# Performance work log

Hardware: AMD Instinct MI355X
Metric: run time of the kernel (lower is better)

The kernel has to match this reference:

```python
import jax, jax.numpy as jnp
import numpy as np

DIM = 1024
DEPTH = 2
HEADS = 16
DH = 64
INNER = HEADS * DH  # == DIM
MLP = 4096
B, N, M = 2, 1024, 1024
EPS = 1e-5
SCALE = DH ** -0.5


def _ln(x, g, b):
    mu = x.mean(-1, keepdims=True)
    var = ((x - mu) ** 2).mean(-1, keepdims=True)
    return (x - mu) / jnp.sqrt(var + EPS) * g + b


def _split_heads(t):  # [b, n, inner] -> [b, h, n, d]
    b, n, _ = t.shape
    return t.reshape(b, n, HEADS, DH).transpose(0, 2, 1, 3)


def _merge_heads(t):  # [b, h, n, d] -> [b, n, inner]
    b, h, n, d = t.shape
    return t.transpose(0, 2, 1, 3).reshape(b, n, h * d)


def _mha(q, k, v):
    dots = jnp.einsum('bhnd,bhmd->bhnm', q, k) * SCALE
    attn = jax.nn.softmax(dots, axis=-1)
    return jnp.einsum('bhnm,bhmd->bhnd', attn, v)


def setup_inputs() -> dict:
    key = jax.random.key(0)
    ks = jax.random.split(key, 12)
    rn = lambda k, shape, s=0.02: jax.random.normal(k, shape, dtype=jnp.float32) * s
    return {
        'x': rn(ks[0], (B, N, DIM), 1.0),
        'context': rn(ks[1], (B, M, DIM), 1.0),
        'ln1_g': jnp.ones((DEPTH, DIM), jnp.float32),
        'ln1_b': jnp.zeros((DEPTH, DIM), jnp.float32),
        'w_qkv': rn(ks[2], (DEPTH, DIM, 3 * INNER)),
        'w_o1': rn(ks[3], (DEPTH, INNER, DIM)),
        'b_o1': jnp.zeros((DEPTH, DIM), jnp.float32),
        'ln2_g': jnp.ones((DEPTH, DIM), jnp.float32),
        'ln2_b': jnp.zeros((DEPTH, DIM), jnp.float32),
        'w_q': rn(ks[4], (DEPTH, DIM, INNER)),
        'w_k': rn(ks[5], (DEPTH, DIM, INNER)),
        'w_v': rn(ks[6], (DEPTH, DIM, INNER)),
        'w_o2': rn(ks[7], (DEPTH, INNER, DIM)),
        'b_o2': jnp.zeros((DEPTH, DIM), jnp.float32),
        'ln3_g': jnp.ones((DEPTH, DIM), jnp.float32),
        'ln3_b': jnp.zeros((DEPTH, DIM), jnp.float32),
        'w_ff1': rn(ks[8], (DEPTH, DIM, MLP)),
        'b_ff1': jnp.zeros((DEPTH, MLP), jnp.float32),
        'w_ff2': rn(ks[9], (DEPTH, MLP, DIM)),
        'b_ff2': jnp.zeros((DEPTH, DIM), jnp.float32),
    }


def reference(x, context, ln1_g, ln1_b, w_qkv, w_o1, b_o1, ln2_g, ln2_b,
              w_q, w_k, w_v, w_o2, b_o2, ln3_g, ln3_b,
              w_ff1, b_ff1, w_ff2, b_ff2):
    for l in range(DEPTH):
        # PreNorm self-attention + residual
        h = _ln(x, ln1_g[l], ln1_b[l])
        qkv = h @ w_qkv[l]
        q, k, v = jnp.split(qkv, 3, axis=-1)
        out = _merge_heads(_mha(_split_heads(q), _split_heads(k), _split_heads(v)))
        x = out @ w_o1[l] + b_o1[l] + x
        # PreNorm cross-attention (context is NOT normed, matching PreNorm) + residual
        h = _ln(x, ln2_g[l], ln2_b[l])
        q2 = _split_heads(h @ w_q[l])
        k2 = _split_heads(context @ w_k[l])
        v2 = _split_heads(context @ w_v[l])
        out = _merge_heads(_mha(q2, k2, v2))
        x = out @ w_o2[l] + b_o2[l] + x
        # PreNorm FFN (exact GELU, matching nn.GELU default) + residual
        h = _ln(x, ln3_g[l], ln3_b[l])
        h = jax.nn.gelu(h @ w_ff1[l] + b_ff1[l], approximate=False)
        x = h @ w_ff2[l] + b_ff2[l] + x
    return x
```

## Files before the change

### kernel.cpp

```cpp
#include <hip/hip_runtime.h>

typedef __attribute__((ext_vector_type(8))) short bf16x8;
typedef __attribute__((ext_vector_type(4))) short short4v;
typedef __attribute__((ext_vector_type(4))) float f32x4;

__device__ __forceinline__ float bf2f(short s) {
    union { unsigned u; float f; } c;
    c.u = ((unsigned)(unsigned short)s) << 16;
    return c.f;
}
__device__ __forceinline__ short f2bf(float f) {
    union { float f; unsigned u; } c; c.f = f;
    unsigned r = (c.u + 0x7fffu + ((c.u >> 16) & 1u)) >> 16;
    return (short)r;
}

#define AS1(p) ((__attribute__((address_space(1))) void*)(void*)(p))
#define AS3(p) ((__attribute__((address_space(3))) void*)(p))

template<int MODE, int BM>
__global__ __launch_bounds__(256) void gemm_bt(
    const short* __restrict__ A, int lda,
    const short* __restrict__ B, int ldb,
    void* __restrict__ Cv, int ldc,
    const float* __restrict__ bias, const float* __restrict__ resid,
    int M, int N, int K, int ntn, float scale)
{
    constexpr int MF = (BM == 128) ? 4 : 2;
    __shared__ short As[BM * 32];
    __shared__ short Bs[128 * 32];

    const int tm = (blockIdx.x / ntn) * BM;
    const int tn = (blockIdx.x % ntn) * 128;

    const int tid = threadIdx.x;
    const int w = tid >> 6, l = tid & 63;
    const int lane16 = l & 15, kg = l >> 4;
    const int wr = (BM == 128) ? (w >> 1) * 64 : (w & 1) * 32;
    const int wc = (BM == 128) ? (w & 1) * 64 : (w >> 1) * 64;

    f32x4 acc[MF][4] = {};

    for (int k0 = 0; k0 < K; k0 += 32) {
        if constexpr (BM == 128) {
            const int lr = l >> 2, lc = l & 3;
            #pragma unroll
            for (int i = 0; i < 2; ++i) {
                int row = (i * 4 + w) * 16 + lr;
                int ga = tm + row; if (ga > M - 1) ga = M - 1;
                const short* srca = A + (long)ga * lda + k0 + lc * 8;
                __builtin_amdgcn_global_load_lds(AS1(srca), AS3(As + (i * 4 + w) * 512), 16, 0, 0);
                int gb = tn + row; if (gb > N - 1) gb = N - 1;
                const short* srcb = B + (long)gb * ldb + k0 + lc * 8;
                __builtin_amdgcn_global_load_lds(AS1(srcb), AS3(Bs + (i * 4 + w) * 512), 16, 0, 0);
            }
        } else {
            const int lr = l >> 2, lc = l & 3;
            {
                int row = w * 16 + lr;
                int ga = tm + row; if (ga > M - 1) ga = M - 1;
                const short* srca = A + (long)ga * lda + k0 + lc * 8;
                __builtin_amdgcn_global_load_lds(AS1(srca), AS3(As + w * 512), 16, 0, 0);
            }
            #pragma unroll
            for (int i = 0; i < 2; ++i) {
                int row = i * 64 + w * 16 + lr;
                int gb = tn + row; if (gb > N - 1) gb = N - 1;
                const short* srcb = B + (long)gb * ldb + k0 + lc * 8;
                __builtin_amdgcn_global_load_lds(AS1(srcb), AS3(Bs + i * 2048 + w * 512), 16, 0, 0);
            }
        }
        __syncthreads();

        bf16x8 af[MF], bfr[4];
        #pragma unroll
        for (int m = 0; m < MF; ++m)
            af[m] = *(const bf16x8*)(As + (wr + m * 16 + lane16) * 32 + kg * 8);
        #pragma unroll
        for (int n = 0; n < 4; ++n)
            bfr[n] = *(const bf16x8*)(Bs + (wc + n * 16 + lane16) * 32 + kg * 8);
        #pragma unroll
        for (int m = 0; m < MF; ++m)
            #pragma unroll
            for (int n = 0; n < 4; ++n)
                acc[m][n] = __builtin_amdgcn_mfma_f32_16x16x32_bf16(af[m], bfr[n], acc[m][n], 0, 0, 0);
        __syncthreads();
    }

    if (MODE == 2) {
        float* C = (float*)Cv;
        #pragma unroll
        for (int m = 0; m < MF; ++m)
            #pragma unroll
            for (int n = 0; n < 4; ++n) {
                int col = tn + wc + n * 16 + lane16;
                if (col >= N) continue;
                #pragma unroll
                for (int r = 0; r < 4; ++r) {
                    int row = tm + wr + m * 16 + kg * 4 + r;
                    if (row >= M) continue;
                    long idx = (long)row * ldc + col;
                    C[idx] = acc[m][n][r] * scale + bias[col] + resid[idx];
                }
            }
    } else {
        short* C = (short*)Cv;
        #pragma unroll
        for (int m = 0; m < MF; ++m)
            #pragma unroll
            for (int n = 0; n < 4; ++n) {
                int col = tn + wc + n * 16 + lane16;
                if (col >= N) continue;
                #pragma unroll
                for (int r = 0; r < 4; ++r) {
                    int row = tm + wr + m * 16 + kg * 4 + r;
                    if (row >= M) continue;
                    float v = acc[m][n][r] * scale;
                    if (MODE == 1) {
                        v += bias[col];
                        v = 0.5f * v * (1.0f + erff(v * 0.7071067811865476f));
                    }
                    C[(long)row * ldc + col] = f2bf(v);
                }
            }
    }
}

__global__ __launch_bounds__(512) void flash_attn(
    const short* __restrict__ Q, int ldq, long sQb,
    const short* __restrict__ K, int ldk, long sKb,
    const short* __restrict__ Vt,
    short* __restrict__ O, int ldo, long sOb)
{
    __shared__ short Ks[2][64 * 64];
    __shared__ short Vts[2][64 * 64];
    __shared__ short Ps[8][16 * 72];

    const int z = blockIdx.x;
    const int b = z >> 4, h = z & 15;
    const int qt = blockIdx.y;

    const int tid = threadIdx.x;
    const int w = tid >> 6, l = tid & 63;
    const int lane16 = l & 15, kg = l >> 4;

    const short* Qg = Q + sQb * b + h * 64;
    const short* Kg = K + sKb * b + h * 64;
    const short* Vtg = Vt + (long)z * 65536;
    short* Og = O + sOb * b + h * 64 + (long)(qt * 128 + w * 16) * ldo;

    const int srow = w * 8 + (l >> 3);
    const int schunk = (l & 7) ^ (srow & 7);

    bf16x8 aq[2];
    {
        const short* qp = Qg + (long)(qt * 128 + w * 16 + lane16) * ldq + kg * 8;
        aq[0] = *(const bf16x8*)(qp);
        aq[1] = *(const bf16x8*)(qp + 32);
    }

    f32x4 acc_o[4] = {};
    float m_run[4], l_run[4];
    #pragma unroll
    for (int r = 0; r < 4; ++r) { m_run[r] = -1e30f; l_run[r] = 0.f; }

    short* Pw = (short*)Ps + w * (16 * 72);

    {
        const short* srck = Kg + (long)srow * ldk + schunk * 8;
        __builtin_amdgcn_global_load_lds(AS1(srck), AS3((short*)Ks + w * 512), 16, 0, 0);
        const short* srcv = Vtg + (long)srow * 1024 + schunk * 8;
        __builtin_amdgcn_global_load_lds(AS1(srcv), AS3((short*)Vts + w * 512), 16, 0, 0);
    }

    int cur = 0;
    for (int t = 0; t < 16; ++t) {
        __syncthreads();
        if (t < 15) {
            const short* srck = Kg + (long)((t + 1) * 64 + srow) * ldk + schunk * 8;
            __builtin_amdgcn_global_load_lds(AS1(srck), AS3((short*)Ks + (cur ^ 1) * 4096 + w * 512), 16, 0, 0);
            const short* srcv = Vtg + (long)srow * 1024 + (t + 1) * 64 + schunk * 8;
            __builtin_amdgcn_global_load_lds(AS1(srcv), AS3((short*)Vts + (cur ^ 1) * 4096 + w * 512), 16, 0, 0);
        }
        const short* Kb = (const short*)Ks + cur * 4096;
        const short* Vb = (const short*)Vts + cur * 4096;

        f32x4 acc_s[4] = {};
        #pragma unroll
        for (int n = 0; n < 4; ++n) {
            int row = 16 * n + lane16;
            #pragma unroll
            for (int ks = 0; ks < 2; ++ks) {
                bf16x8 bk = *(const bf16x8*)(Kb + row * 64 + (((ks * 4 + kg) ^ (row & 7)) * 8));
                acc_s[n] = __builtin_amdgcn_mfma_f32_16x16x32_bf16(aq[ks], bk, acc_s[n], 0, 0, 0);
            }
        }

        float mt[4], p[4][4], rs[4], mnew[4], corr[4];
        #pragma unroll
        for (int n = 0; n < 4; ++n)
            #pragma unroll
            for (int r = 0; r < 4; ++r) acc_s[n][r] *= 0.125f;
        #pragma unroll
        for (int r = 0; r < 4; ++r)
            mt[r] = fmaxf(fmaxf(acc_s[0][r], acc_s[1][r]), fmaxf(acc_s[2][r], acc_s[3][r]));
        #pragma unroll
        for (int off = 1; off < 16; off <<= 1)
            #pragma unroll
            for (int r = 0; r < 4; ++r) mt[r] = fmaxf(mt[r], __shfl_xor(mt[r], off));
        #pragma unroll
        for (int r = 0; r < 4; ++r) {
            mnew[r] = fmaxf(m_run[r], mt[r]);
            corr[r] = __expf(m_run[r] - mnew[r]);
            m_run[r] = mnew[r];
            rs[r] = 0.f;
        }
        #pragma unroll
        for (int n = 0; n < 4; ++n)
            #pragma unroll
            for (int r = 0; r < 4; ++r) {
                float e = __expf(acc_s[n][r] - mnew[r]);
                p[n][r] = e; rs[r] += e;
            }
        #pragma unroll
        for (int off = 1; off < 16; off <<= 1)
            #pragma unroll
            for (int r = 0; r < 4; ++r) rs[r] += __shfl_xor(rs[r], off);
        #pragma unroll
        for (int r = 0; r < 4; ++r) {
            l_run[r] = l_run[r] * corr[r] + rs[r];
            #pragma unroll
            for (int nd = 0; nd < 4; ++nd) acc_o[nd][r] *= corr[r];
        }

        #pragma unroll
        for (int n = 0; n < 4; ++n)
            #pragma unroll
            for (int r = 0; r < 4; ++r)
                Pw[(kg * 4 + r) * 72 + 16 * n + lane16] = f2bf(p[n][r]);

        #pragma unroll
        for (int kk = 0; kk < 2; ++kk) {
            bf16x8 pa = *(const bf16x8*)(Pw + lane16 * 72 + kk * 32 + kg * 8);
            #pragma unroll
            for (int nd = 0; nd < 4; ++nd) {
                int d = 16 * nd + lane16;
                bf16x8 bv = *(const bf16x8*)(Vb + d * 64 + (((kk * 4 + kg) ^ (d & 7)) * 8));
                acc_o[nd] = __builtin_amdgcn_mfma_f32_16x16x32_bf16(pa, bv, acc_o[nd], 0, 0, 0);
            }
        }
        cur ^= 1;
    }

    #pragma unroll
    for (int r = 0; r < 4; ++r) {
        float inv = 1.0f / l_run[r];
        #pragma unroll
        for (int nd = 0; nd < 4; ++nd)
            Og[(long)(kg * 4 + r) * ldo + nd * 16 + lane16] = f2bf(acc_o[nd][r] * inv);
    }
}

__global__ __launch_bounds__(256) void ln_bf16(const float* __restrict__ x,
                                               const float* __restrict__ g,
                                               const float* __restrict__ b,
                                               short* __restrict__ h)
{
    const long row = blockIdx.x;
    const int tid = threadIdx.x;
    float4 v = ((const float4*)(x + row * 1024))[tid];
    float s  = v.x + v.y + v.z + v.w;
    float s2 = v.x * v.x + v.y * v.y + v.z * v.z + v.w * v.w;
    #pragma unroll
    for (int off = 1; off < 64; off <<= 1) {
        s  += __shfl_xor(s, off);
        s2 += __shfl_xor(s2, off);
    }
    __shared__ float rs[4], rs2[4];
    int w = tid >> 6;
    if ((tid & 63) == 0) { rs[w] = s; rs2[w] = s2; }
    __syncthreads();
    s  = rs[0] + rs[1] + rs[2] + rs[3];
    s2 = rs2[0] + rs2[1] + rs2[2] + rs2[3];
    float mu  = s * (1.0f / 1024.0f);
    float var = s2 * (1.0f / 1024.0f) - mu * mu;
    float inv = rsqrtf(var + 1e-5f);
    float4 gv = ((const float4*)g)[tid];
    float4 bv = ((const float4*)b)[tid];
    short4v o;
    o[0] = f2bf((v.x - mu) * inv * gv.x + bv.x);
    o[1] = f2bf((v.y - mu) * inv * gv.y + bv.y);
    o[2] = f2bf((v.z - mu) * inv * gv.z + bv.z);
    o[3] = f2bf((v.w - mu) * inv * gv.w + bv.w);
    ((short4v*)(h + row * 1024))[tid] = o;
}

__global__ __launch_bounds__(256) void wconv_t(const float* __restrict__ in,
                                               short* __restrict__ out, int R, int C)
{
    __shared__ float t[32][33];
    const int c0 = blockIdx.x * 32, r0 = blockIdx.y * 32;
    const int tx = threadIdx.x & 31, ty = threadIdx.x >> 5;
    #pragma unroll
    for (int i = 0; i < 4; ++i)
        t[ty + i * 8][tx] = in[(long)(r0 + ty + i * 8) * C + c0 + tx];
    __syncthreads();
    #pragma unroll
    for (int i = 0; i < 4; ++i)
        out[(long)(c0 + ty + i * 8) * R + r0 + tx] = f2bf(t[tx][ty + i * 8]);
}

__global__ __launch_bounds__(256) void vtrans(const short* __restrict__ src, int ld, int col_off,
                                              short* __restrict__ vt)
{
    __shared__ short t[32][33];
    const int z = blockIdx.z, bb = z >> 4, hh = z & 15;
    const int m0 = blockIdx.x * 32, d0 = blockIdx.y * 32;
    const int tx = threadIdx.x & 31, ty = threadIdx.x >> 5;
    const short* sp = src + (long)(bb * 1024) * ld + col_off + hh * 64;
    #pragma unroll
    for (int i = 0; i < 4; ++i)
        t[ty + i * 8][tx] = sp[(long)(m0 + ty + i * 8) * ld + d0 + tx];
    __syncthreads();
    short* op = vt + (long)z * 64 * 1024;
    #pragma unroll
    for (int i = 0; i < 4; ++i)
        op[(long)(d0 + ty + i * 8) * 1024 + m0 + tx] = t[tx][ty + i * 8];
}

__global__ __launch_bounds__(256) void f2bf_vec(const float* __restrict__ in,
                                                short* __restrict__ out, int n4)
{
    int i = blockIdx.x * 256 + threadIdx.x;
    if (i < n4) {
        float4 v = ((const float4*)in)[i];
        short4v o;
        o[0] = f2bf(v.x); o[1] = f2bf(v.y); o[2] = f2bf(v.z); o[3] = f2bf(v.w);
        ((short4v*)out)[i] = o;
    }
}

template<int MODE, int BM>
static void launch_gemm(const short* A, int lda, const short* B, int ldb,
                        void* C, int ldc, const float* bias, const float* resid,
                        int M, int N, int K, float scale, hipStream_t stream)
{
    int ntm = (M + BM - 1) / BM, ntn = (N + 127) / 128;
    dim3 grid(ntm * ntn);
    gemm_bt<MODE, BM><<<grid, 256, 0, stream>>>(A, lda, B, ldb, C, ldc, bias, resid,
                                                M, N, K, ntn, scale);
}

extern "C" void kernel_launch(void* const* d_in, const int* in_sizes, int n_in,
                              void* d_out, int out_size, void* d_ws, size_t ws_size,
                              hipStream_t stream)
{
    const float* x_in  = (const float*)d_in[0];
    const float* ctx   = (const float*)d_in[1];
    const float* ln1_g = (const float*)d_in[2];
    const float* ln1_b = (const float*)d_in[3];
    const float* w_qkv = (const float*)d_in[4];
    const float* w_o1  = (const float*)d_in[5];
    const float* b_o1  = (const float*)d_in[6];
    const float* ln2_g = (const float*)d_in[7];
    const float* ln2_b = (const float*)d_in[8];
    const float* w_q   = (const float*)d_in[9];
    const float* w_k   = (const float*)d_in[10];
    const float* w_v   = (const float*)d_in[11];
    const float* w_o2  = (const float*)d_in[12];
    const float* b_o2  = (const float*)d_in[13];
    const float* ln3_g = (const float*)d_in[14];
    const float* ln3_b = (const float*)d_in[15];
    const float* w_ff1 = (const float*)d_in[16];
    const float* b_ff1 = (const float*)d_in[17];
    const float* w_ff2 = (const float*)d_in[18];
    const float* b_ff2 = (const float*)d_in[19];
    float* xo = (float*)d_out;

    char* p = (char*)d_ws;
    short* wbuf   = (short*)(p);
    short* hbuf   = (short*)(p + 8388608);
    short* qkvbuf = (short*)(p + 12582912);
    short* vt     = (short*)(p + 92274688);
    short* aout   = (short*)(p + 96468992);
    short* ffbuf  = (short*)(p + 100663296);
    short* ctxbuf = (short*)(p + 117440512);

    hipMemcpyAsync(xo, x_in, (size_t)2 * 1024 * 1024 * 4, hipMemcpyDeviceToDevice, stream);
    f2bf_vec<<<2048, 256, 0, stream>>>(ctx, ctxbuf, 2 * 1024 * 1024 / 4);

    for (int l = 0; l < 2; ++l) {
        ln_bf16<<<2048, 256, 0, stream>>>(xo, ln1_g + l * 1024, ln1_b + l * 1024, hbuf);
        wconv_t<<<dim3(96, 32), 256, 0, stream>>>(w_qkv + (long)l * 1024 * 3072, wbuf, 1024, 3072);
        launch_gemm<0, 128>(hbuf, 1024, wbuf, 1024, qkvbuf, 3072,
                            nullptr, nullptr, 2048, 3072, 1024, 1.0f, stream);
        vtrans<<<dim3(32, 2, 32), 256, 0, stream>>>(qkvbuf, 3072, 2048, vt);
        flash_attn<<<dim3(32, 8), 512, 0, stream>>>(qkvbuf, 3072, 3145728L,
                                                    qkvbuf + 1024, 3072, 3145728L,
                                                    vt, aout, 1024, 1048576L);
        wconv_t<<<dim3(32, 32), 256, 0, stream>>>(w_o1 + (long)l * 1048576, wbuf, 1024, 1024);
        launch_gemm<2, 64>(aout, 1024, wbuf, 1024, xo, 1024,
                           b_o1 + l * 1024, xo, 2048, 1024, 1024, 1.0f, stream);

        ln_bf16<<<2048, 256, 0, stream>>>(xo, ln2_g + l * 1024, ln2_b + l * 1024, hbuf);
        short* q2 = qkvbuf;
        short* k2 = qkvbuf + 2048 * 1024;
        short* v2 = qkvbuf + 2 * 2048 * 1024;
        wconv_t<<<dim3(32, 32), 256, 0, stream>>>(w_q + (long)l * 1048576, wbuf, 1024, 1024);
        launch_gemm<0, 64>(hbuf, 1024, wbuf, 1024, q2, 1024,
                           nullptr, nullptr, 2048, 1024, 1024, 1.0f, stream);
        wconv_t<<<dim3(32, 32), 256, 0, stream>>>(w_k + (long)l * 1048576, wbuf, 1024, 1024);
        launch_gemm<0, 64>(ctxbuf, 1024, wbuf, 1024, k2, 1024,
                           nullptr, nullptr, 2048, 1024, 1024, 1.0f, stream);
        wconv_t<<<dim3(32, 32), 256, 0, stream>>>(w_v + (long)l * 1048576, wbuf, 1024, 1024);
        launch_gemm<0, 64>(ctxbuf, 1024, wbuf, 1024, v2, 1024,
                           nullptr, nullptr, 2048, 1024, 1024, 1.0f, stream);
        vtrans<<<dim3(32, 2, 32), 256, 0, stream>>>(v2, 1024, 0, vt);
        flash_attn<<<dim3(32, 8), 512, 0, stream>>>(q2, 1024, 1048576L,
                                                    k2, 1024, 1048576L,
                                                    vt, aout, 1024, 1048576L);
        wconv_t<<<dim3(32, 32), 256, 0, stream>>>(w_o2 + (long)l * 1048576, wbuf, 1024, 1024);
        launch_gemm<2, 64>(aout, 1024, wbuf, 1024, xo, 1024,
                           b_o2 + l * 1024, xo, 2048, 1024, 1024, 1.0f, stream);

        ln_bf16<<<2048, 256, 0, stream>>>(xo, ln3_g + l * 1024, ln3_b + l * 1024, hbuf);
        wconv_t<<<dim3(128, 32), 256, 0, stream>>>(w_ff1 + (long)l * 1024 * 4096, wbuf, 1024, 4096);
        launch_gemm<1, 128>(hbuf, 1024, wbuf, 1024, ffbuf, 4096,
                            b_ff1 + l * 4096, nullptr, 2048, 4096, 1024, 1.0f, stream);
        wconv_t<<<dim3(32, 128), 256, 0, stream>>>(w_ff2 + (long)l * 4096 * 1024, wbuf, 4096, 1024);
        launch_gemm<2, 64>(ffbuf, 4096, wbuf, 4096, xo, 1024,
                           b_ff2 + l * 1024, xo, 2048, 1024, 4096, 1.0f, stream);
    }
}
```

Baseline: 910.5 us.

## Rewrite GEMM with triple-buffered async LDS pipeline, swizzle, and fused K/V projection

Replaces the single-buffered GEMM with a three-stage LDS ring fed by global_load_lds. Each stage covers K=64 and uses an XOR swizzle to avoid bank conflicts. Explicit vmcnt waits let loads for stage t+2 overlap compute on stage t, and block IDs are remapped for L2 locality. The cross-attention K and V projections are merged into one GEMM with N=2048 writing an interleaved buffer. Bounds checks are removed, so all dimensions must now be exact multiples of the tile sizes.

```diff
diff --git a/kernel.cpp b/kernel.cpp
--- a/kernel.cpp
+++ b/kernel.cpp
@@ -19,19 +19,24 @@
 #define AS3(p) ((__attribute__((address_space(3))) void*)(p))
 
 template<int MODE, int BM>
-__global__ __launch_bounds__(256) void gemm_bt(
+__global__ __launch_bounds__(256) void gemm2(
     const short* __restrict__ A, int lda,
     const short* __restrict__ B, int ldb,
     void* __restrict__ Cv, int ldc,
     const float* __restrict__ bias, const float* __restrict__ resid,
-    int M, int N, int K, int ntn, float scale)
+    int ntn, int nt, float scale)
 {
     constexpr int MF = (BM == 128) ? 4 : 2;
-    __shared__ short As[BM * 32];
-    __shared__ short Bs[128 * 32];
-
-    const int tm = (blockIdx.x / ntn) * BM;
-    const int tn = (blockIdx.x % ntn) * 128;
+    constexpr int NIA = BM / 32;
+    __shared__ short As[3][BM * 64];
+    __shared__ short Bs[3][128 * 64];
+
+    const int nwg = gridDim.x;
+    const int bid = blockIdx.x;
+    const int tile = (bid & 7) * (nwg >> 3) + (bid >> 3);
+
+    const int tm = (tile / ntn) * BM;
+    const int tn = (tile % ntn) * 128;
 
     const int tid = threadIdx.x;
     const int w = tid >> 6, l = tid & 63;
@@ -39,53 +44,78 @@
     const int wr = (BM == 128) ? (w >> 1) * 64 : (w & 1) * 32;
     const int wc = (BM == 128) ? (w & 1) * 64 : (w >> 1) * 64;
 
+    const short* pa[NIA];
+    const short* pb[4];
+    #pragma unroll
+    for (int j = 0; j < NIA; ++j) {
+        int row = (j * 4 + w) * 8 + (l >> 3);
+        pa[j] = A + (long)(tm + row) * lda + (((l & 7) ^ (row & 7)) * 8);
+    }
+    #pragma unroll
+    for (int j = 0; j < 4; ++j) {
+        int row = (j * 4 + w) * 8 + (l >> 3);
+        pb[j] = B + (long)(tn + row) * ldb + (((l & 7) ^ (row & 7)) * 8);
+    }
+
     f32x4 acc[MF][4] = {};
 
-    for (int k0 = 0; k0 < K; k0 += 32) {
-        if constexpr (BM == 128) {
-            const int lr = l >> 2, lc = l & 3;
-            #pragma unroll
-            for (int i = 0; i < 2; ++i) {
-                int row = (i * 4 + w) * 16 + lr;
-                int ga = tm + row; if (ga > M - 1) ga = M - 1;
-                const short* srca = A + (long)ga * lda + k0 + lc * 8;
-                __builtin_amdgcn_global_load_lds(AS1(srca), AS3(As + (i * 4 + w) * 512), 16, 0, 0);
-                int gb = tn + row; if (gb > N - 1) gb = N - 1;
-                const short* srcb = B + (long)gb * ldb + k0 + lc * 8;
-                __builtin_amdgcn_global_load_lds(AS1(srcb), AS3(Bs + (i * 4 + w) * 512), 16, 0, 0);
-            }
-        } else {
-            const int lr = l >> 2, lc = l & 3;
-            {
-                int row = w * 16 + lr;
-                int ga = tm + row; if (ga > M - 1) ga = M - 1;
-                const short* srca = A + (long)ga * lda + k0 + lc * 8;
-                __builtin_amdgcn_global_load_lds(AS1(srca), AS3(As + w * 512), 16, 0, 0);
-            }
-            #pragma unroll
-            for (int i = 0; i < 2; ++i) {
-                int row = i * 64 + w * 16 + lr;
-                int gb = tn + row; if (gb > N - 1) gb = N - 1;
-                const short* srcb = B + (long)gb * ldb + k0 + lc * 8;
-                __builtin_amdgcn_global_load_lds(AS1(srcb), AS3(Bs + i * 2048 + w * 512), 16, 0, 0);
-            }
-        }
-        __syncthreads();
-
-        bf16x8 af[MF], bfr[4];
-        #pragma unroll
-        for (int m = 0; m < MF; ++m)
-            af[m] = *(const bf16x8*)(As + (wr + m * 16 + lane16) * 32 + kg * 8);
-        #pragma unroll
-        for (int n = 0; n < 4; ++n)
-            bfr[n] = *(const bf16x8*)(Bs + (wc + n * 16 + lane16) * 32 + kg * 8);
-        #pragma unroll
-        for (int m = 0; m < MF; ++m)
+    auto stage = [&](int buf) {
+        #pragma unroll
+        for (int j = 0; j < NIA; ++j) {
+            __builtin_amdgcn_global_load_lds(AS1(pa[j]), AS3(&As[buf][(j * 4 + w) * 512]), 16, 0, 0);
+            pa[j] += 64;
+        }
+        #pragma unroll
+        for (int j = 0; j < 4; ++j) {
+            __builtin_amdgcn_global_load_lds(AS1(pb[j]), AS3(&Bs[buf][(j * 4 + w) * 512]), 16, 0, 0);
+            pb[j] += 64;
+        }
+    };
+
+    auto compute = [&](int buf) {
+        bf16x8 af[2][MF], bfr[2][4];
+        #pragma unroll
+        for (int kk = 0; kk < 2; ++kk) {
+            int swz = ((kk * 4 + kg) ^ (lane16 & 7)) * 8;
+            #pragma unroll
+            for (int m = 0; m < MF; ++m)
+                af[kk][m] = *(const bf16x8*)&As[buf][(wr + m * 16 + lane16) * 64 + swz];
             #pragma unroll
             for (int n = 0; n < 4; ++n)
-                acc[m][n] = __builtin_amdgcn_mfma_f32_16x16x32_bf16(af[m], bfr[n], acc[m][n], 0, 0, 0);
-        __syncthreads();
-    }
+                bfr[kk][n] = *(const bf16x8*)&Bs[buf][(wc + n * 16 + lane16) * 64 + swz];
+        }
+        #pragma unroll
+        for (int kk = 0; kk < 2; ++kk)
+            #pragma unroll
+            for (int m = 0; m < MF; ++m)
+                #pragma unroll
+                for (int n = 0; n < 4; ++n)
+                    acc[m][n] = __builtin_amdgcn_mfma_f32_16x16x32_bf16(af[kk][m], bfr[kk][n], acc[m][n], 0, 0, 0);
+    };
+
+    #define WAIT_VMCNT_L()  do { \
+        if constexpr (BM == 64) asm volatile("s_waitcnt vmcnt(6)" ::: "memory"); \
+        else                    asm volatile("s_waitcnt vmcnt(8)" ::: "memory"); \
+        __builtin_amdgcn_sched_barrier(0); \
+        __builtin_amdgcn_s_barrier(); \
+        __builtin_amdgcn_sched_barrier(0); } while (0)
+
+    stage(0);
+    stage(1);
+    WAIT_VMCNT_L();
+
+    for (int t = 0; t < nt - 2; ++t) {
+        stage((t + 2) % 3);
+        compute(t % 3);
+        WAIT_VMCNT_L();
+    }
+    compute((nt - 2) % 3);
+    asm volatile("s_waitcnt vmcnt(0)" ::: "memory");
+    __builtin_amdgcn_sched_barrier(0);
+    __builtin_amdgcn_s_barrier();
+    __builtin_amdgcn_sched_barrier(0);
+    compute((nt - 1) % 3);
+    #undef WAIT_VMCNT_L
 
     if (MODE == 2) {
         float* C = (float*)Cv;
@@ -94,11 +124,9 @@
             #pragma unroll
             for (int n = 0; n < 4; ++n) {
                 int col = tn + wc + n * 16 + lane16;
-                if (col >= N) continue;
                 #pragma unroll
                 for (int r = 0; r < 4; ++r) {
                     int row = tm + wr + m * 16 + kg * 4 + r;
-                    if (row >= M) continue;
                     long idx = (long)row * ldc + col;
                     C[idx] = acc[m][n][r] * scale + bias[col] + resid[idx];
                 }
@@ -110,11 +138,9 @@
             #pragma unroll
             for (int n = 0; n < 4; ++n) {
                 int col = tn + wc + n * 16 + lane16;
-                if (col >= N) continue;
                 #pragma unroll
                 for (int r = 0; r < 4; ++r) {
                     int row = tm + wr + m * 16 + kg * 4 + r;
-                    if (row >= M) continue;
                     float v = acc[m][n][r] * scale;
                     if (MODE == 1) {
                         v += bias[col];
@@ -341,14 +367,13 @@
 }
 
 template<int MODE, int BM>
-static void launch_gemm(const short* A, int lda, const short* B, int ldb,
-                        void* C, int ldc, const float* bias, const float* resid,
-                        int M, int N, int K, float scale, hipStream_t stream)
-{
-    int ntm = (M + BM - 1) / BM, ntn = (N + 127) / 128;
-    dim3 grid(ntm * ntn);
-    gemm_bt<MODE, BM><<<grid, 256, 0, stream>>>(A, lda, B, ldb, C, ldc, bias, resid,
-                                                M, N, K, ntn, scale);
+static void launch_gemm2(const short* A, int lda, const short* B, int ldb,
+                         void* C, int ldc, const float* bias, const float* resid,
+                         int M, int N, int K, hipStream_t stream)
+{
+    int ntm = M / BM, ntn = N / 128;
+    gemm2<MODE, BM><<<dim3(ntm * ntn), 256, 0, stream>>>(A, lda, B, ldb, C, ldc,
+                                                         bias, resid, ntn, K / 64, 1.0f);
 }
 
 extern "C" void kernel_launch(void* const* d_in, const int* in_sizes, int n_in,
@@ -381,6 +406,7 @@
     short* wbuf   = (short*)(p);
     short* hbuf   = (short*)(p + 8388608);
     short* qkvbuf = (short*)(p + 12582912);
+    short* k2v2   = (short*)(p + 25165824);
     short* vt     = (short*)(p + 92274688);
     short* aout   = (short*)(p + 96468992);
     short* ffbuf  = (short*)(p + 100663296);
@@ -392,43 +418,39 @@
     for (int l = 0; l < 2; ++l) {
         ln_bf16<<<2048, 256, 0, stream>>>(xo, ln1_g + l * 1024, ln1_b + l * 1024, hbuf);
         wconv_t<<<dim3(96, 32), 256, 0, stream>>>(w_qkv + (long)l * 1024 * 3072, wbuf, 1024, 3072);
-        launch_gemm<0, 128>(hbuf, 1024, wbuf, 1024, qkvbuf, 3072,
-                            nullptr, nullptr, 2048, 3072, 1024, 1.0f, stream);
+        launch_gemm2<0, 128>(hbuf, 1024, wbuf, 1024, qkvbuf, 3072,
+                             nullptr, nullptr, 2048, 3072, 1024, stream);
         vtrans<<<dim3(32, 2, 32), 256, 0, stream>>>(qkvbuf, 3072, 2048, vt);
         flash_attn<<<dim3(32, 8), 512, 0, stream>>>(qkvbuf, 3072, 3145728L,
                                                     qkvbuf + 1024, 3072, 3145728L,
                                                     vt, aout, 1024, 1048576L);
         wconv_t<<<dim3(32, 32), 256, 0, stream>>>(w_o1 + (long)l * 1048576, wbuf, 1024, 1024);
-        launch_gemm<2, 64>(aout, 1024, wbuf, 1024, xo, 1024,
-                           b_o1 + l * 1024, xo, 2048, 1024, 1024, 1.0f, stream);
+        launch_gemm2<2, 64>(aout, 1024, wbuf, 1024, xo, 1024,
+                            b_o1 + l * 1024, xo, 2048, 1024, 1024, stream);
 
         ln_bf16<<<2048, 256, 0, stream>>>(xo, ln2_g + l * 1024, ln2_b + l * 1024, hbuf);
         short* q2 = qkvbuf;
-        short* k2 = qkvbuf + 2048 * 1024;
-        short* v2 = qkvbuf + 2 * 2048 * 1024;
         wconv_t<<<dim3(32, 32), 256, 0, stream>>>(w_q + (long)l * 1048576, wbuf, 1024, 1024);
-        launch_gemm<0, 64>(hbuf, 1024, wbuf, 1024, q2, 1024,
-                           nullptr, nullptr, 2048, 1024, 1024, 1.0f, stream);
+        launch_gemm2<0, 64>(hbuf, 1024, wbuf, 1024, q2, 1024,
+                            nullptr, nullptr, 2048, 1024, 1024, stream);
         wconv_t<<<dim3(32, 32), 256, 0, stream>>>(w_k + (long)l * 1048576, wbuf, 1024, 1024);
-        launch_gemm<0, 64>(ctxbuf, 1024, wbuf, 1024, k2, 1024,
-                           nullptr, nullptr, 2048, 1024, 1024, 1.0f, stream);
-        wconv_t<<<dim3(32, 32), 256, 0, stream>>>(w_v + (long)l * 1048576, wbuf, 1024, 1024);
-        launch_gemm<0, 64>(ctxbuf, 1024, wbuf, 1024, v2, 1024,
-                           nullptr, nullptr, 2048, 1024, 1024, 1.0f, stream);
-        vtrans<<<dim3(32, 2, 32), 256, 0, stream>>>(v2, 1024, 0, vt);
+        wconv_t<<<dim3(32, 32), 256, 0, stream>>>(w_v + (long)l * 1048576, wbuf + 1048576, 1024, 1024);
+        launch_gemm2<0, 64>(ctxbuf, 1024, wbuf, 1024, k2v2, 2048,
+                            nullptr, nullptr, 2048, 2048, 1024, stream);
+        vtrans<<<dim3(32, 2, 32), 256, 0, stream>>>(k2v2 + 1024, 2048, 0, vt);
         flash_attn<<<dim3(32, 8), 512, 0, stream>>>(q2, 1024, 1048576L,
-                                                    k2, 1024, 1048576L,
+                                                    k2v2, 2048, 2097152L,
                                                     vt, aout, 1024, 1048576L);
         wconv_t<<<dim3(32, 32), 256, 0, stream>>>(w_o2 + (long)l * 1048576, wbuf, 1024, 1024);
-        launch_gemm<2, 64>(aout, 1024, wbuf, 1024, xo, 1024,
-                           b_o2 + l * 1024, xo, 2048, 1024, 1024, 1.0f, stream);
+        launch_gemm2<2, 64>(aout, 1024, wbuf, 1024, xo, 1024,
+                            b_o2 + l * 1024, xo, 2048, 1024, 1024, stream);
 
         ln_bf16<<<2048, 256, 0, stream>>>(xo, ln3_g + l * 1024, ln3_b + l * 1024, hbuf);
         wconv_t<<<dim3(128, 32), 256, 0, stream>>>(w_ff1 + (long)l * 1024 * 4096, wbuf, 1024, 4096);
-        launch_gemm<1, 128>(hbuf, 1024, wbuf, 1024, ffbuf, 4096,
-                            b_ff1 + l * 4096, nullptr, 2048, 4096, 1024, 1.0f, stream);
+        launch_gemm2<1, 128>(hbuf, 1024, wbuf, 1024, ffbuf, 4096,
+                             b_ff1 + l * 4096, nullptr, 2048, 4096, 1024, stream);
         wconv_t<<<dim3(32, 128), 256, 0, stream>>>(w_ff2 + (long)l * 4096 * 1024, wbuf, 4096, 1024);
-        launch_gemm<2, 64>(ffbuf, 4096, wbuf, 4096, xo, 1024,
-                           b_ff2 + l * 1024, xo, 2048, 1024, 4096, 1.0f, stream);
-    }
-}
+        launch_gemm2<2, 64>(ffbuf, 4096, wbuf, 4096, xo, 1024,
+                            b_ff2 + l * 1024, xo, 2048, 1024, 4096, stream);
+    }
+}
```

Measured after the change: 876.7 us. -3.7%, faster.
